# Performance work log

Measured on AMD Instinct MI355X. Metric: run time of the kernel, lower is better.

Reference implementation:

```python
import jax, jax.numpy as jnp
import numpy as np

B, P, H, W = 8, 24, 448, 448
NUM_CLS = 19
DISK_R2 = 25.0  # (5 ** 2) hardcoded threshold in the original


def setup_inputs() -> dict:
    key = jax.random.key(0)
    k1, k2, k3, k4 = jax.random.split(key, 4)
    x = jax.random.normal(k1, (B, 3, H, W), dtype=jnp.float32)
    # (row, col) click coordinates in-range, class id in [0, 19)
    rc = jax.random.randint(k2, (B, P, 2), 0, H).astype(jnp.float32)
    cls = jax.random.randint(k3, (B, P, 1), 0, NUM_CLS).astype(jnp.float32)
    invalid = jax.random.uniform(k4, (B, P, 1)) < 0.1
    rc = jnp.where(invalid, -1.0, rc)
    coords = jnp.concatenate([rc, cls], axis=-1)  # [B, P, 3]
    return {"x": x, "coords": coords}


def reference(x, coords):
    b, _, h, w = x.shape
    p = coords.shape[1]
    pts = coords[..., :2]                      # [B,P,2] (row, col)
    cls = coords[..., 2].astype(jnp.int32)     # [B,P]
    # invalid if max(row, col) < 0 (original sets dist to 1e6 -> mask False)
    valid = jnp.max(pts, axis=-1) >= 0         # [B,P]

    rows = jnp.arange(h, dtype=coords.dtype)
    cols = jnp.arange(w, dtype=coords.dtype)
    dr = rows[None, None, :, None] - pts[..., 0][..., None, None]  # [B,P,H,1]
    dc = cols[None, None, None, :] - pts[..., 1][..., None, None]  # [B,P,1,W]
    d2 = dr * dr + dc * dc                     # [B,P,H,W]
    mask = ((d2 <= DISK_R2) & valid[..., None, None]).astype(x.dtype)  # [B,P,H,W]

    # scatter each point's disk into its class channel, max-reduce over points
    bidx = jnp.broadcast_to(jnp.arange(b)[:, None], (b, p))  # [B,P]
    res = jnp.zeros((b, NUM_CLS, h, w), x.dtype).at[bidx, cls].max(mask)
    return res * 255.0
```

## Files before the change

kernel.cpp:

```cpp
#include <hip/hip_runtime.h>

#define B_SZ 8
#define P_SZ 24
#define H_SZ 448
#define W_SZ 448
#define HWPIX (H_SZ * W_SZ)
#define NUM_CLS 19

__global__ void zero_kernel(float4* __restrict__ out, int n4) {
    int i = blockIdx.x * blockDim.x + threadIdx.x;
    int stride = gridDim.x * blockDim.x;
    float4 z = make_float4(0.f, 0.f, 0.f, 0.f);
    for (; i < n4; i += stride) out[i] = z;
}

__global__ void paint_kernel(const float* __restrict__ coords, float* __restrict__ out) {
    int bp = blockIdx.x;
    int b = bp / P_SZ;
    const float* c = coords + (size_t)bp * 3;
    float rf = c[0], cf = c[1];
    if (fmaxf(rf, cf) < 0.0f) return;
    int cls = (int)c[2];
    int row = (int)rf, col = (int)cf;

    int t = threadIdx.x;
    if (t >= 121) return;
    int dy = t / 11 - 5;
    int dx = t % 11 - 5;
    if (dy * dy + dx * dx > 25) return;
    int y = row + dy;
    int x = col + dx;
    if ((unsigned)y >= (unsigned)H_SZ || (unsigned)x >= (unsigned)W_SZ) return;
    out[((size_t)b * NUM_CLS + cls) * HWPIX + (size_t)y * W_SZ + x] = 255.0f;
}

extern "C" void kernel_launch(void* const* d_in, const int* in_sizes, int n_in,
                              void* d_out, int out_size, void* d_ws, size_t ws_size,
                              hipStream_t stream) {
    const float* coords = (const float*)d_in[1];
    float* out = (float*)d_out;

    int n4 = out_size / 4;
    zero_kernel<<<2048, 256, 0, stream>>>((float4*)out, n4);
    paint_kernel<<<B_SZ * P_SZ, 128, 0, stream>>>(coords, out);
}
```

Before: 26.34 us.

## Fuse zero-fill and disk painting into one per-channel distance-map kernel

```diff
diff --git a/kernel.cpp b/kernel.cpp
--- a/kernel.cpp
+++ b/kernel.cpp
@@ -4,43 +4,75 @@
 #define P_SZ 24
 #define H_SZ 448
 #define W_SZ 448
-#define HWPIX (H_SZ * W_SZ)
 #define NUM_CLS 19
+#define W4 (W_SZ / 4)
+#define CH4 (H_SZ * W_SZ / 4)
+#define THREADS 256
+#define F4_PER_THREAD 2
+#define CHUNK4 (THREADS * F4_PER_THREAD)
+#define BLOCKS_PER_CH (CH4 / CHUNK4)
 
-__global__ void zero_kernel(float4* __restrict__ out, int n4) {
-    int i = blockIdx.x * blockDim.x + threadIdx.x;
-    int stride = gridDim.x * blockDim.x;
-    float4 z = make_float4(0.f, 0.f, 0.f, 0.f);
-    for (; i < n4; i += stride) out[i] = z;
-}
+__global__ __launch_bounds__(THREADS) void fused_distmap_kernel(
+        const float* __restrict__ coords, float4* __restrict__ out) {
+    int ch = blockIdx.x / BLOCKS_PER_CH;
+    int chunk = blockIdx.x % BLOCKS_PER_CH;
+    int b = ch / NUM_CLS;
+    int cls = ch % NUM_CLS;
 
-__global__ void paint_kernel(const float* __restrict__ coords, float* __restrict__ out) {
-    int bp = blockIdx.x;
-    int b = bp / P_SZ;
-    const float* c = coords + (size_t)bp * 3;
-    float rf = c[0], cf = c[1];
-    if (fmaxf(rf, cf) < 0.0f) return;
-    int cls = (int)c[2];
-    int row = (int)rf, col = (int)cf;
+    __shared__ float s_r[P_SZ];
+    __shared__ float s_c[P_SZ];
+    __shared__ int s_cnt;
+    if (threadIdx.x == 0) s_cnt = 0;
+    __syncthreads();
+    if (threadIdx.x < P_SZ) {
+        const float* c = coords + ((size_t)b * P_SZ + threadIdx.x) * 3;
+        float rf = c[0], cf = c[1];
+        int pcls = (int)c[2];
+        if (pcls == cls && fmaxf(rf, cf) >= 0.0f) {
+            int slot = atomicAdd(&s_cnt, 1);
+            s_r[slot] = rf;
+            s_c[slot] = cf;
+        }
+    }
+    __syncthreads();
+    int cnt = s_cnt;
 
-    int t = threadIdx.x;
-    if (t >= 121) return;
-    int dy = t / 11 - 5;
-    int dx = t % 11 - 5;
-    if (dy * dy + dx * dx > 25) return;
-    int y = row + dy;
-    int x = col + dx;
-    if ((unsigned)y >= (unsigned)H_SZ || (unsigned)x >= (unsigned)W_SZ) return;
-    out[((size_t)b * NUM_CLS + cls) * HWPIX + (size_t)y * W_SZ + x] = 255.0f;
+    size_t chbase = (size_t)ch * CH4;
+    int idx0 = chunk * CHUNK4 + threadIdx.x;
+
+    if (cnt == 0) {
+        float4 z = make_float4(0.f, 0.f, 0.f, 0.f);
+        #pragma unroll
+        for (int u = 0; u < F4_PER_THREAD; ++u)
+            out[chbase + idx0 + u * THREADS] = z;
+        return;
+    }
+
+    #pragma unroll
+    for (int u = 0; u < F4_PER_THREAD; ++u) {
+        int idx4 = idx0 + u * THREADS;
+        float y  = (float)(idx4 / W4);
+        float x0 = (float)((idx4 % W4) * 4);
+        float4 v = make_float4(0.f, 0.f, 0.f, 0.f);
+        for (int p = 0; p < cnt; ++p) {
+            float dr  = y - s_r[p];
+            float dr2 = dr * dr;
+            float dc  = x0 - s_c[p];
+            if (dr2 + dc * dc                   <= 25.f) v.x = 255.f;
+            if (dr2 + (dc+1.f) * (dc+1.f)       <= 25.f) v.y = 255.f;
+            if (dr2 + (dc+2.f) * (dc+2.f)       <= 25.f) v.z = 255.f;
+            if (dr2 + (dc+3.f) * (dc+3.f)       <= 25.f) v.w = 255.f;
+        }
+        out[chbase + idx4] = v;
+    }
 }
 
 extern "C" void kernel_launch(void* const* d_in, const int* in_sizes, int n_in,
                               void* d_out, int out_size, void* d_ws, size_t ws_size,
                               hipStream_t stream) {
     const float* coords = (const float*)d_in[1];
-    float* out = (float*)d_out;
+    float4* out = (float4*)d_out;
 
-    int n4 = out_size / 4;
-    zero_kernel<<<2048, 256, 0, stream>>>((float4*)out, n4);
-    paint_kernel<<<B_SZ * P_SZ, 128, 0, stream>>>(coords, out);
+    int grid = B_SZ * NUM_CLS * BLOCKS_PER_CH;
+    fused_distmap_kernel<<<grid, THREADS, 0, stream>>>(coords, out);
 }
```

New measurement: 21.87 us. 17.0% less time.
